# Optimization experiments

Measured on AMD Instinct MI355X. Metric: run time of the kernel, lower is better.

Reference implementation:

```python
import jax, jax.numpy as jnp
import numpy as np

N_NODES = 50000
N_EDGES = 1600000
IN_FEAT = 128
HEADS = 8
OUT_FEAT = 16


def setup_inputs() -> dict:
    key = jax.random.key(0)
    ks = jax.random.split(key, 8)
    feat = jax.random.normal(ks[0], (N_NODES, IN_FEAT), dtype=jnp.float32)
    src = jax.random.randint(ks[1], (N_EDGES,), 0, N_NODES, dtype=jnp.int32)
    dst = jax.random.randint(ks[2], (N_EDGES,), 0, N_NODES, dtype=jnp.int32)
    eps = jax.random.normal(ks[3], (N_EDGES, HEADS), dtype=jnp.float32)
    # small init scale keeps exp(log_scale) numerically tame
    W_fc = jax.random.normal(ks[4], (IN_FEAT, HEADS * OUT_FEAT), dtype=jnp.float32) * 0.05
    W_post = jax.random.normal(ks[5], (OUT_FEAT, 4), dtype=jnp.float32) * 0.05
    b_post = jax.random.normal(ks[6], (4,), dtype=jnp.float32) * 0.05
    bias = jax.random.normal(ks[7], (HEADS, OUT_FEAT), dtype=jnp.float32) * 0.05
    return {"feat": feat, "src": src, "dst": dst, "eps": eps,
            "W_fc": W_fc, "W_post": W_post, "b_post": b_post, "bias": bias}


def reference(feat, src, dst, eps, W_fc, W_post, b_post, bias):
    N = feat.shape[0]
    # node projection: [N, H, F]
    h = (feat @ W_fc).reshape(N, HEADS, OUT_FEAT)
    # per-node posterior params: [N, H, 4] -> loc_l, loc_r, log_scale_l, log_scale_r
    post = jnp.einsum('nhf,fk->nhk', h, W_post) + b_post
    loc_l, loc_r, lsl, lsr = post[..., 0], post[..., 1], post[..., 2], post[..., 3]
    # per-edge score via reparameterized sample: [E, H]
    loc = loc_l[src] + loc_r[dst]
    log_scale = lsl[src] + lsr[dst]
    e = loc + jnp.exp(log_scale) * eps
    # edge softmax over incoming edges of each dst node (per head)
    m = jax.lax.stop_gradient(jax.ops.segment_max(e, dst, num_segments=N))
    ex = jnp.exp(e - m[dst])
    denom = jax.ops.segment_sum(ex, dst, num_segments=N)
    a = ex / denom[dst]
    # weighted aggregation: sum over in-edges of h[src] * a
    msg = h[src] * a[:, :, None]                     # [E, H, F]
    out = jax.ops.segment_sum(msg, dst, num_segments=N)  # [N, H, F]
    out = out + bias[None]
    return out
```

## Files before the change

kernel.cpp:

```cpp
#include <hip/hip_runtime.h>
#include <hip/hip_fp16.h>

#define IN_FEAT 128
#define HEADS 8
#define OUT_FEAT 16
#define HF 128
#define BSHIFT 6
#define BNODES 64
#define NBMAX 1024
#define CHUNK 8192

__global__ __launch_bounds__(256) void gemm_post_kernel(
    const float* __restrict__ feat, const float* __restrict__ W_fc,
    const float* __restrict__ W_post, const float* __restrict__ b_post,
    __half* __restrict__ hbuf, float* __restrict__ post, int N)
{
    __shared__ float4 lds4[32 * 32];
    float* lds = (float*)lds4;
    const int tid = threadIdx.x;
    const int node_base = blockIdx.x * 32;

    const float4* f4 = (const float4*)feat;
    for (int i = tid; i < 32 * 32; i += 256) {
        int n = i >> 5, k4 = i & 31;
        int gn = node_base + n;
        float4 v = make_float4(0.f, 0.f, 0.f, 0.f);
        if (gn < N) v = f4[gn * 32 + k4];
        lds4[i] = v;
    }
    __syncthreads();

    const int cg = tid & 31, ng = tid >> 5;
    const int n0 = ng * 4;
    float acc[4][4];
#pragma unroll
    for (int i = 0; i < 4; i++) acc[i][0] = acc[i][1] = acc[i][2] = acc[i][3] = 0.f;

    const float4* W4 = (const float4*)W_fc;
#pragma unroll 4
    for (int k = 0; k < 128; ++k) {
        float4 w = W4[k * 32 + cg];
#pragma unroll
        for (int i = 0; i < 4; i++) {
            float f = lds[(n0 + i) * 128 + k];
            acc[i][0] += f * w.x; acc[i][1] += f * w.y;
            acc[i][2] += f * w.z; acc[i][3] += f * w.w;
        }
    }
    __half2* hb2 = (__half2*)hbuf;
#pragma unroll
    for (int i = 0; i < 4; i++) {
        int gn = node_base + n0 + i;
        if (gn < N) {
            union { uint2 u; __half2 h[2]; } pk;
            pk.h[0] = __floats2half2_rn(acc[i][0], acc[i][1]);
            pk.h[1] = __floats2half2_rn(acc[i][2], acc[i][3]);
            *(uint2*)&hb2[gn * 64 + cg * 2] = pk.u;
        }
    }
    __syncthreads();
#pragma unroll
    for (int i = 0; i < 4; i++)
        lds4[(n0 + i) * 32 + cg] = make_float4(acc[i][0], acc[i][1], acc[i][2], acc[i][3]);
    __syncthreads();

    {
        int n = tid >> 3, h = tid & 7;
        float p0 = b_post[0], p1 = b_post[1], p2 = b_post[2], p3 = b_post[3];
#pragma unroll
        for (int f = 0; f < 16; ++f) {
            float v = lds[n * 128 + h * 16 + f];
            p0 += v * W_post[f * 4 + 0];
            p1 += v * W_post[f * 4 + 1];
            p2 += v * W_post[f * 4 + 2];
            p3 += v * W_post[f * 4 + 3];
        }
        int gn = node_base + n;
        if (gn < N) {
            post[gn * 32 + 0 * 8 + h] = p0;
            post[gn * 32 + 1 * 8 + h] = p1;
            post[gn * 32 + 2 * 8 + h] = p2;
            post[gn * 32 + 3 * 8 + h] = p3;
        }
    }
}

__global__ __launch_bounds__(256) void bucket_hist_kernel(
    const int* __restrict__ dst, int* __restrict__ bucket_tot, int E, int nb)
{
    __shared__ int cnt[NBMAX];
    const int tid = threadIdx.x;
    for (int i = tid; i < nb; i += 256) cnt[i] = 0;
    __syncthreads();
    const int stride = gridDim.x * 256;
    for (int g = blockIdx.x * 256 + tid; g < E; g += stride)
        atomicAdd(&cnt[dst[g] >> BSHIFT], 1);
    __syncthreads();
    for (int i = tid; i < nb; i += 256) {
        int c = cnt[i];
        if (c) atomicAdd(&bucket_tot[i], c);
    }
}

__global__ __launch_bounds__(256) void bucket_scan_kernel(
    const int* __restrict__ bucket_tot, int* __restrict__ bucket_base,
    int* __restrict__ bucket_cursor, int nb, int E)
{
    __shared__ int sd[256];
    const int tid = threadIdx.x;
    int v[4]; int s = 0;
#pragma unroll
    for (int k = 0; k < 4; ++k) {
        int i = tid * 4 + k;
        v[k] = (i < nb) ? bucket_tot[i] : 0;
        s += v[k];
    }
    sd[tid] = s;
    __syncthreads();
    for (int off = 1; off < 256; off <<= 1) {
        int t = (tid >= off) ? sd[tid - off] : 0;
        __syncthreads();
        sd[tid] += t;
        __syncthreads();
    }
    int excl = sd[tid] - s;
#pragma unroll
    for (int k = 0; k < 4; ++k) {
        int i = tid * 4 + k;
        if (i < nb) { bucket_base[i] = excl; bucket_cursor[i] = excl; }
        excl += v[k];
    }
    if (tid == 0) bucket_base[nb] = E;
}

__global__ __launch_bounds__(256) void bucket_scatter_kernel(
    const int* __restrict__ src, const int* __restrict__ dst,
    int* __restrict__ bucket_cursor, uint2* __restrict__ recs, int E, int nb)
{
    __shared__ int cnt[NBMAX];
    __shared__ int base[NBMAX];
    const int tid = threadIdx.x;
    for (int i = tid; i < nb; i += 256) cnt[i] = 0;
    __syncthreads();
    const int e0 = blockIdx.x * CHUNK;
    const int e1 = min(e0 + CHUNK, E);
    for (int e = e0 + tid; e < e1; e += 256)
        atomicAdd(&cnt[dst[e] >> BSHIFT], 1);
    __syncthreads();
    for (int i = tid; i < nb; i += 256) {
        int c = cnt[i];
        base[i] = c ? atomicAdd(&bucket_cursor[i], c) : 0;
        cnt[i] = 0;
    }
    __syncthreads();
    for (int e = e0 + tid; e < e1; e += 256) {
        int d = dst[e];
        int b = d >> BSHIFT;
        int slot = base[b] + atomicAdd(&cnt[b], 1);
        recs[slot] = make_uint2((unsigned)e,
                                ((unsigned)src[e] << BSHIFT) | (unsigned)(d & (BNODES - 1)));
    }
}

__global__ __launch_bounds__(256) void bucket_csr_kernel(
    const uint2* __restrict__ recs, const int* __restrict__ bucket_base,
    int* __restrict__ offsets, uint2* __restrict__ csr, int N, int E)
{
    __shared__ int ncnt[BNODES];
    __shared__ int snc[BNODES];
    const int b = blockIdx.x, tid = threadIdx.x;
    const int node_lo = b << BSHIFT;
    const int rlo = bucket_base[b], rhi = bucket_base[b + 1];
    const int gn = node_lo + tid;

    if (tid < BNODES) ncnt[tid] = 0;
    __syncthreads();
    for (int r = rlo + tid; r < rhi; r += 256)
        atomicAdd(&ncnt[recs[r].y & (BNODES - 1u)], 1);
    __syncthreads();
    if (tid < BNODES) snc[tid] = ncnt[tid];
    __syncthreads();
    for (int off = 1; off < BNODES; off <<= 1) {
        int t = (tid < BNODES && tid >= off) ? snc[tid - off] : 0;
        __syncthreads();
        if (tid < BNODES) snc[tid] += t;
        __syncthreads();
    }
    int excl = (tid < BNODES) ? snc[tid] - ncnt[tid] : 0;
    if (tid < BNODES && gn < N) offsets[gn] = rlo + excl;
    if (b == 0 && tid == 0) offsets[N] = E;
    __syncthreads();
    if (tid < BNODES) ncnt[tid] = excl;
    __syncthreads();

    for (int r = rlo + tid; r < rhi; r += 256) {
        uint2 rec = recs[r];
        int dl = (int)(rec.y & (BNODES - 1u));
        unsigned s = rec.y >> BSHIFT;
        int slot = rlo + atomicAdd(&ncnt[dl], 1);
        csr[slot] = make_uint2(rec.x, s);
    }
}

__global__ __launch_bounds__(256) void agg_kernel(
    const uint2* __restrict__ csr, const int* __restrict__ offsets,
    const float* __restrict__ post, const float* __restrict__ eps,
    const __half* __restrict__ hbuf, const float* __restrict__ bias,
    float* __restrict__ out, int N)
{
    const int lane = threadIdx.x & 63;
    const int d = blockIdx.x * 4 + (threadIdx.x >> 6);
    if (d >= N) return;
    const int start = offsets[d];
    const int deg = offsets[d + 1] - start;
    const int j = lane >> 3, hh = lane & 7;
    const int h = j;
    const float dl  = post[d * 32 + 8 + hh];
    const float dls = post[d * 32 + 24 + hh];

    float2 acc = make_float2(0.f, 0.f);
    float dsum = 0.f;

    int c = 0;
    for (; c + 8 <= deg; c += 8) {
        uint2 rec = csr[start + c + j];
        int e = (int)rec.x, s = (int)rec.y;
        float ll = post[s * 32 + hh];
        float sl = post[s * 32 + 16 + hh];
        float ep = eps[(size_t)e * 8 + hh];
        float ex = __expf((ll + dl) + __expf(sl + dls) * ep);
#pragma unroll
        for (int jj = 0; jj < 8; ++jj) {
            float a = __shfl(ex, jj * 8 + h, 64);
            int  sj = __shfl(s, jj * 8, 64);
            float2 hv = __half22float2(((const __half2*)(hbuf + (size_t)sj * HF))[lane]);
            acc.x += a * hv.x;
            acc.y += a * hv.y;
            dsum += a;
        }
    }
    if (c < deg) {
        int jc = deg - c;
        uint2 rec = csr[start + c + min(j, jc - 1)];
        int e = (int)rec.x, s = (int)rec.y;
        float ll = post[s * 32 + hh];
        float sl = post[s * 32 + 16 + hh];
        float ep = eps[(size_t)e * 8 + hh];
        float ex = (j < jc) ? __expf((ll + dl) + __expf(sl + dls) * ep) : 0.f;
        for (int jj = 0; jj < jc; ++jj) {
            float a = __shfl(ex, jj * 8 + h, 64);
            int  sj = __shfl(s, jj * 8, 64);
            float2 hv = __half22float2(((const __half2*)(hbuf + (size_t)sj * HF))[lane]);
            acc.x += a * hv.x;
            acc.y += a * hv.y;
            dsum += a;
        }
    }

    float inv = (dsum > 0.f) ? 1.f / dsum : 0.f;
    float2 bv = ((const float2*)bias)[lane];
    float2 o = make_float2(acc.x * inv + bv.x, acc.y * inv + bv.y);
    ((float2*)out)[(size_t)d * 64 + lane] = o;
}

extern "C" void kernel_launch(void* const* d_in, const int* in_sizes, int n_in,
                              void* d_out, int out_size, void* d_ws, size_t ws_size,
                              hipStream_t stream)
{
    const float* feat   = (const float*)d_in[0];
    const int*   src    = (const int*)d_in[1];
    const int*   dst    = (const int*)d_in[2];
    const float* eps    = (const float*)d_in[3];
    const float* W_fc   = (const float*)d_in[4];
    const float* W_post = (const float*)d_in[5];
    const float* b_post = (const float*)d_in[6];
    const float* bias   = (const float*)d_in[7];
    float* out = (float*)d_out;

    const int N = in_sizes[0] / IN_FEAT;
    const int E = in_sizes[1];
    const int nb = (N + BNODES - 1) >> BSHIFT;

    char* p = (char*)d_ws;
    auto alloc = [&](size_t bytes) {
        char* r = p;
        p += (bytes + 255) & ~size_t(255);
        return r;
    };
    __half* hbuf    = (__half*)alloc((size_t)N * HF * 2);
    float*  post    = (float*)alloc((size_t)N * 32 * 4);
    int*    offsets = (int*)alloc((size_t)(N + 1) * 4);
    int*    bucket_tot    = (int*)alloc((size_t)(NBMAX + 1) * 4);
    int*    bucket_base   = (int*)alloc((size_t)(NBMAX + 1) * 4);
    int*    bucket_cursor = (int*)alloc((size_t)(NBMAX + 1) * 4);
    uint2*  recs    = (uint2*)alloc((size_t)E * 8);
    uint2*  csr     = (uint2*)alloc((size_t)E * 8);

    hipMemsetAsync(bucket_tot, 0, (size_t)nb * 4, stream);

    gemm_post_kernel<<<(N + 31) / 32, 256, 0, stream>>>(feat, W_fc, W_post, b_post,
                                                        hbuf, post, N);
    bucket_hist_kernel<<<512, 256, 0, stream>>>(dst, bucket_tot, E, nb);
    bucket_scan_kernel<<<1, 256, 0, stream>>>(bucket_tot, bucket_base,
                                              bucket_cursor, nb, E);
    bucket_scatter_kernel<<<(E + CHUNK - 1) / CHUNK, 256, 0, stream>>>(
        src, dst, bucket_cursor, recs, E, nb);
    bucket_csr_kernel<<<nb, 256, 0, stream>>>(recs, bucket_base, offsets, csr, N, E);
    agg_kernel<<<(N + 3) / 4, 256, 0, stream>>>(csr, offsets, post, eps, hbuf,
                                                bias, out, N);
}
```

Baseline: 333.4 us.

## Fuse GEMM with bucket scatter and sort per-bucket edges inside aggregation

Runs the edge bucket scatter and the node projection GEMM as disjoint block ranges of a single launch, so the two independent jobs overlap. It drops the separate CSR-building kernel. The aggregation kernel now takes one 64-node bucket per block, builds a local permutation of that bucket's records in shared memory, and accumulates all 8 nodes per wave in registers. This avoids writing and re-reading a full CSR array and saves a launch, at the cost of more shared memory, a larger register footprint, and fewer, heavier aggregation blocks that may load-balance poorly.

```diff
diff --git a/kernel.cpp b/kernel.cpp
--- a/kernel.cpp
+++ b/kernel.cpp
@@ -8,17 +8,96 @@
 #define BSHIFT 6
 #define BNODES 64
 #define NBMAX 1024
-#define CHUNK 8192
-
-__global__ __launch_bounds__(256) void gemm_post_kernel(
+#define CHUNK 4096
+#define PCAP 4096
+
+__global__ __launch_bounds__(256) void bucket_hist_kernel(
+    const int* __restrict__ dst, int* __restrict__ bucket_tot, int E, int nb)
+{
+    __shared__ int cnt[NBMAX];
+    const int tid = threadIdx.x;
+    for (int i = tid; i < nb; i += 256) cnt[i] = 0;
+    __syncthreads();
+    const int stride = gridDim.x * 256;
+    for (int g = blockIdx.x * 256 + tid; g < E; g += stride)
+        atomicAdd(&cnt[dst[g] >> BSHIFT], 1);
+    __syncthreads();
+    for (int i = tid; i < nb; i += 256) {
+        int c = cnt[i];
+        if (c) atomicAdd(&bucket_tot[i], c);
+    }
+}
+
+__global__ __launch_bounds__(256) void bucket_scan_kernel(
+    const int* __restrict__ bucket_tot, int* __restrict__ bucket_base,
+    int* __restrict__ bucket_cursor, int nb, int E)
+{
+    __shared__ int sd[256];
+    const int tid = threadIdx.x;
+    int v[4]; int s = 0;
+#pragma unroll
+    for (int k = 0; k < 4; ++k) {
+        int i = tid * 4 + k;
+        v[k] = (i < nb) ? bucket_tot[i] : 0;
+        s += v[k];
+    }
+    sd[tid] = s;
+    __syncthreads();
+    for (int off = 1; off < 256; off <<= 1) {
+        int t = (tid >= off) ? sd[tid - off] : 0;
+        __syncthreads();
+        sd[tid] += t;
+        __syncthreads();
+    }
+    int excl = sd[tid] - s;
+#pragma unroll
+    for (int k = 0; k < 4; ++k) {
+        int i = tid * 4 + k;
+        if (i < nb) { bucket_base[i] = excl; bucket_cursor[i] = excl; }
+        excl += v[k];
+    }
+    if (tid == 0) bucket_base[nb] = E;
+}
+
+__global__ __launch_bounds__(256) void gemm_scatter_kernel(
     const float* __restrict__ feat, const float* __restrict__ W_fc,
     const float* __restrict__ W_post, const float* __restrict__ b_post,
-    __half* __restrict__ hbuf, float* __restrict__ post, int N)
+    __half* __restrict__ hbuf, float* __restrict__ post, int N,
+    const int* __restrict__ src, const int* __restrict__ dst,
+    int* __restrict__ bucket_cursor, uint2* __restrict__ recs, int E, int nb,
+    int SB)
 {
     __shared__ float4 lds4[32 * 32];
+    const int tid = threadIdx.x;
+
+    if (blockIdx.x < SB) {
+        int* cnt  = (int*)lds4;
+        int* base = cnt + NBMAX;
+        for (int i = tid; i < nb; i += 256) cnt[i] = 0;
+        __syncthreads();
+        const int e0 = blockIdx.x * CHUNK;
+        const int e1 = min(e0 + CHUNK, E);
+        for (int e = e0 + tid; e < e1; e += 256)
+            atomicAdd(&cnt[dst[e] >> BSHIFT], 1);
+        __syncthreads();
+        for (int i = tid; i < nb; i += 256) {
+            int c = cnt[i];
+            base[i] = c ? atomicAdd(&bucket_cursor[i], c) : 0;
+            cnt[i] = 0;
+        }
+        __syncthreads();
+        for (int e = e0 + tid; e < e1; e += 256) {
+            int d = dst[e];
+            int b = d >> BSHIFT;
+            int slot = base[b] + atomicAdd(&cnt[b], 1);
+            recs[slot] = make_uint2((unsigned)e,
+                                    ((unsigned)src[e] << BSHIFT) | (unsigned)(d & (BNODES - 1)));
+        }
+        return;
+    }
+
     float* lds = (float*)lds4;
-    const int tid = threadIdx.x;
-    const int node_base = blockIdx.x * 32;
+    const int node_base = (blockIdx.x - SB) * 32;
 
     const float4* f4 = (const float4*)feat;
     for (int i = tid; i < 32 * 32; i += 256) {
@@ -85,182 +164,120 @@
     }
 }
 
-__global__ __launch_bounds__(256) void bucket_hist_kernel(
-    const int* __restrict__ dst, int* __restrict__ bucket_tot, int E, int nb)
-{
-    __shared__ int cnt[NBMAX];
-    const int tid = threadIdx.x;
-    for (int i = tid; i < nb; i += 256) cnt[i] = 0;
-    __syncthreads();
-    const int stride = gridDim.x * 256;
-    for (int g = blockIdx.x * 256 + tid; g < E; g += stride)
-        atomicAdd(&cnt[dst[g] >> BSHIFT], 1);
-    __syncthreads();
-    for (int i = tid; i < nb; i += 256) {
-        int c = cnt[i];
-        if (c) atomicAdd(&bucket_tot[i], c);
-    }
-}
-
-__global__ __launch_bounds__(256) void bucket_scan_kernel(
-    const int* __restrict__ bucket_tot, int* __restrict__ bucket_base,
-    int* __restrict__ bucket_cursor, int nb, int E)
-{
-    __shared__ int sd[256];
-    const int tid = threadIdx.x;
-    int v[4]; int s = 0;
-#pragma unroll
-    for (int k = 0; k < 4; ++k) {
-        int i = tid * 4 + k;
-        v[k] = (i < nb) ? bucket_tot[i] : 0;
-        s += v[k];
-    }
-    sd[tid] = s;
-    __syncthreads();
-    for (int off = 1; off < 256; off <<= 1) {
-        int t = (tid >= off) ? sd[tid - off] : 0;
-        __syncthreads();
-        sd[tid] += t;
-        __syncthreads();
-    }
-    int excl = sd[tid] - s;
-#pragma unroll
-    for (int k = 0; k < 4; ++k) {
-        int i = tid * 4 + k;
-        if (i < nb) { bucket_base[i] = excl; bucket_cursor[i] = excl; }
-        excl += v[k];
-    }
-    if (tid == 0) bucket_base[nb] = E;
-}
-
-__global__ __launch_bounds__(256) void bucket_scatter_kernel(
-    const int* __restrict__ src, const int* __restrict__ dst,
-    int* __restrict__ bucket_cursor, uint2* __restrict__ recs, int E, int nb)
-{
-    __shared__ int cnt[NBMAX];
-    __shared__ int base[NBMAX];
-    const int tid = threadIdx.x;
-    for (int i = tid; i < nb; i += 256) cnt[i] = 0;
-    __syncthreads();
-    const int e0 = blockIdx.x * CHUNK;
-    const int e1 = min(e0 + CHUNK, E);
-    for (int e = e0 + tid; e < e1; e += 256)
-        atomicAdd(&cnt[dst[e] >> BSHIFT], 1);
-    __syncthreads();
-    for (int i = tid; i < nb; i += 256) {
-        int c = cnt[i];
-        base[i] = c ? atomicAdd(&bucket_cursor[i], c) : 0;
-        cnt[i] = 0;
-    }
-    __syncthreads();
-    for (int e = e0 + tid; e < e1; e += 256) {
-        int d = dst[e];
-        int b = d >> BSHIFT;
-        int slot = base[b] + atomicAdd(&cnt[b], 1);
-        recs[slot] = make_uint2((unsigned)e,
-                                ((unsigned)src[e] << BSHIFT) | (unsigned)(d & (BNODES - 1)));
-    }
-}
-
-__global__ __launch_bounds__(256) void bucket_csr_kernel(
+__global__ __launch_bounds__(512) void agg_kernel(
     const uint2* __restrict__ recs, const int* __restrict__ bucket_base,
-    int* __restrict__ offsets, uint2* __restrict__ csr, int N, int E)
-{
+    const float* __restrict__ post, const float* __restrict__ eps,
+    const __half* __restrict__ hbuf, const float* __restrict__ bias,
+    float* __restrict__ out, int N)
+{
+    __shared__ unsigned short perm[PCAP];
     __shared__ int ncnt[BNODES];
-    __shared__ int snc[BNODES];
+    __shared__ int offs[BNODES];
+    __shared__ int cur[BNODES];
+
     const int b = blockIdx.x, tid = threadIdx.x;
     const int node_lo = b << BSHIFT;
     const int rlo = bucket_base[b], rhi = bucket_base[b + 1];
-    const int gn = node_lo + tid;
-
-    if (tid < BNODES) ncnt[tid] = 0;
-    __syncthreads();
-    for (int r = rlo + tid; r < rhi; r += 256)
-        atomicAdd(&ncnt[recs[r].y & (BNODES - 1u)], 1);
-    __syncthreads();
-    if (tid < BNODES) snc[tid] = ncnt[tid];
-    __syncthreads();
-    for (int off = 1; off < BNODES; off <<= 1) {
-        int t = (tid < BNODES && tid >= off) ? snc[tid - off] : 0;
-        __syncthreads();
-        if (tid < BNODES) snc[tid] += t;
-        __syncthreads();
-    }
-    int excl = (tid < BNODES) ? snc[tid] - ncnt[tid] : 0;
-    if (tid < BNODES && gn < N) offsets[gn] = rlo + excl;
-    if (b == 0 && tid == 0) offsets[N] = E;
-    __syncthreads();
-    if (tid < BNODES) ncnt[tid] = excl;
-    __syncthreads();
-
-    for (int r = rlo + tid; r < rhi; r += 256) {
-        uint2 rec = recs[r];
-        int dl = (int)(rec.y & (BNODES - 1u));
-        unsigned s = rec.y >> BSHIFT;
-        int slot = rlo + atomicAdd(&ncnt[dl], 1);
-        csr[slot] = make_uint2(rec.x, s);
-    }
-}
-
-__global__ __launch_bounds__(256) void agg_kernel(
-    const uint2* __restrict__ csr, const int* __restrict__ offsets,
-    const float* __restrict__ post, const float* __restrict__ eps,
-    const __half* __restrict__ hbuf, const float* __restrict__ bias,
-    float* __restrict__ out, int N)
-{
-    const int lane = threadIdx.x & 63;
-    const int d = blockIdx.x * 4 + (threadIdx.x >> 6);
-    if (d >= N) return;
-    const int start = offsets[d];
-    const int deg = offsets[d + 1] - start;
+    const int T = rhi - rlo;
+    const int w = tid >> 6, lane = tid & 63;
     const int j = lane >> 3, hh = lane & 7;
-    const int h = j;
-    const float dl  = post[d * 32 + 8 + hh];
-    const float dls = post[d * 32 + 24 + hh];
-
-    float2 acc = make_float2(0.f, 0.f);
-    float dsum = 0.f;
-
-    int c = 0;
-    for (; c + 8 <= deg; c += 8) {
-        uint2 rec = csr[start + c + j];
-        int e = (int)rec.x, s = (int)rec.y;
-        float ll = post[s * 32 + hh];
-        float sl = post[s * 32 + 16 + hh];
-        float ep = eps[(size_t)e * 8 + hh];
-        float ex = __expf((ll + dl) + __expf(sl + dls) * ep);
-#pragma unroll
-        for (int jj = 0; jj < 8; ++jj) {
-            float a = __shfl(ex, jj * 8 + h, 64);
-            int  sj = __shfl(s, jj * 8, 64);
-            float2 hv = __half22float2(((const __half2*)(hbuf + (size_t)sj * HF))[lane]);
-            acc.x += a * hv.x;
-            acc.y += a * hv.y;
-            dsum += a;
-        }
-    }
-    if (c < deg) {
-        int jc = deg - c;
-        uint2 rec = csr[start + c + min(j, jc - 1)];
-        int e = (int)rec.x, s = (int)rec.y;
-        float ll = post[s * 32 + hh];
-        float sl = post[s * 32 + 16 + hh];
-        float ep = eps[(size_t)e * 8 + hh];
-        float ex = (j < jc) ? __expf((ll + dl) + __expf(sl + dls) * ep) : 0.f;
-        for (int jj = 0; jj < jc; ++jj) {
-            float a = __shfl(ex, jj * 8 + h, 64);
-            int  sj = __shfl(s, jj * 8, 64);
-            float2 hv = __half22float2(((const __half2*)(hbuf + (size_t)sj * HF))[lane]);
-            acc.x += a * hv.x;
-            acc.y += a * hv.y;
-            dsum += a;
-        }
-    }
-
-    float inv = (dsum > 0.f) ? 1.f / dsum : 0.f;
-    float2 bv = ((const float2*)bias)[lane];
-    float2 o = make_float2(acc.x * inv + bv.x, acc.y * inv + bv.y);
-    ((float2*)out)[(size_t)d * 64 + lane] = o;
+
+    float2 acc[8];
+    float dsum[8];
+#pragma unroll
+    for (int i = 0; i < 8; i++) { acc[i] = make_float2(0.f, 0.f); dsum[i] = 0.f; }
+
+    for (int cb = 0; cb < T; cb += PCAP) {
+        const int Tc = min(PCAP, T - cb);
+        const uint2* rbase = recs + rlo + cb;
+
+        if (tid < BNODES) ncnt[tid] = 0;
+        __syncthreads();
+        for (int r = tid; r < Tc; r += 512)
+            atomicAdd(&ncnt[rbase[r].y & (BNODES - 1u)], 1);
+        __syncthreads();
+        if (tid < 64) {
+            int v = ncnt[tid];
+            int s = v;
+#pragma unroll
+            for (int off = 1; off < 64; off <<= 1) {
+                int t = __shfl_up(s, off, 64);
+                if (lane >= off) s += t;
+            }
+            offs[tid] = s - v;
+            cur[tid]  = s - v;
+        }
+        __syncthreads();
+        for (int r = tid; r < Tc; r += 512) {
+            int dl = (int)(rbase[r].y & (BNODES - 1u));
+            int slot = atomicAdd(&cur[dl], 1);
+            perm[slot] = (unsigned short)r;
+        }
+        __syncthreads();
+
+#pragma unroll
+        for (int i = 0; i < 8; i++) {
+            const int n = (i << 3) | w;
+            const int cn = ncnt[n];
+            if (cn == 0) continue;
+            const int o = offs[n];
+            const int gn = node_lo + n;
+            float dlr = 0.f, dls = 0.f;
+            if (gn < N) { dlr = post[gn * 32 + 8 + hh]; dls = post[gn * 32 + 24 + hh]; }
+
+            int c = 0;
+            for (; c + 8 <= cn; c += 8) {
+                int pidx = perm[o + c + j];
+                uint2 rec = rbase[pidx];
+                int e = (int)rec.x, s = (int)(rec.y >> BSHIFT);
+                float ll = post[s * 32 + hh];
+                float sl = post[s * 32 + 16 + hh];
+                float ep = eps[(size_t)e * 8 + hh];
+                float ex = __expf((ll + dlr) + __expf(sl + dls) * ep);
+#pragma unroll
+                for (int jj = 0; jj < 8; ++jj) {
+                    float a = __shfl(ex, jj * 8 + j, 64);
+                    int  sj = __shfl(s, jj * 8, 64);
+                    float2 hv = __half22float2(((const __half2*)(hbuf + (size_t)sj * HF))[lane]);
+                    acc[i].x += a * hv.x;
+                    acc[i].y += a * hv.y;
+                    dsum[i] += a;
+                }
+            }
+            if (c < cn) {
+                int jc = cn - c;
+                int pidx = perm[o + c + min(j, jc - 1)];
+                uint2 rec = rbase[pidx];
+                int e = (int)rec.x, s = (int)(rec.y >> BSHIFT);
+                float ll = post[s * 32 + hh];
+                float sl = post[s * 32 + 16 + hh];
+                float ep = eps[(size_t)e * 8 + hh];
+                float ex = (j < jc) ? __expf((ll + dlr) + __expf(sl + dls) * ep) : 0.f;
+                for (int jj = 0; jj < jc; ++jj) {
+                    float a = __shfl(ex, jj * 8 + j, 64);
+                    int  sj = __shfl(s, jj * 8, 64);
+                    float2 hv = __half22float2(((const __half2*)(hbuf + (size_t)sj * HF))[lane]);
+                    acc[i].x += a * hv.x;
+                    acc[i].y += a * hv.y;
+                    dsum[i] += a;
+                }
+            }
+        }
+        __syncthreads();
+    }
+
+    const float2 bv = ((const float2*)bias)[lane];
+    float2* out2 = (float2*)out;
+#pragma unroll
+    for (int i = 0; i < 8; i++) {
+        int n = (i << 3) | w;
+        int gn = node_lo + n;
+        if (gn < N) {
+            float inv = (dsum[i] > 0.f) ? 1.f / dsum[i] : 0.f;
+            out2[(size_t)gn * 64 + lane] = make_float2(acc[i].x * inv + bv.x,
+                                                       acc[i].y * inv + bv.y);
+        }
+    }
 }
 
 extern "C" void kernel_launch(void* const* d_in, const int* in_sizes, int n_in,
@@ -280,6 +297,8 @@
     const int N = in_sizes[0] / IN_FEAT;
     const int E = in_sizes[1];
     const int nb = (N + BNODES - 1) >> BSHIFT;
+    const int SB = (E + CHUNK - 1) / CHUNK;
+    const int GB = (N + 31) / 32;
 
     char* p = (char*)d_ws;
     auto alloc = [&](size_t bytes) {
@@ -289,23 +308,19 @@
     };
     __half* hbuf    = (__half*)alloc((size_t)N * HF * 2);
     float*  post    = (float*)alloc((size_t)N * 32 * 4);
-    int*    offsets = (int*)alloc((size_t)(N + 1) * 4);
     int*    bucket_tot    = (int*)alloc((size_t)(NBMAX + 1) * 4);
     int*    bucket_base   = (int*)alloc((size_t)(NBMAX + 1) * 4);
     int*    bucket_cursor = (int*)alloc((size_t)(NBMAX + 1) * 4);
     uint2*  recs    = (uint2*)alloc((size_t)E * 8);
-    uint2*  csr     = (uint2*)alloc((size_t)E * 8);
 
     hipMemsetAsync(bucket_tot, 0, (size_t)nb * 4, stream);
 
-    gemm_post_kernel<<<(N + 31) / 32, 256, 0, stream>>>(feat, W_fc, W_post, b_post,
-                                                        hbuf, post, N);
     bucket_hist_kernel<<<512, 256, 0, stream>>>(dst, bucket_tot, E, nb);
     bucket_scan_kernel<<<1, 256, 0, stream>>>(bucket_tot, bucket_base,
                                               bucket_cursor, nb, E);
-    bucket_scatter_kernel<<<(E + CHUNK - 1) / CHUNK, 256, 0, stream>>>(
-        src, dst, bucket_cursor, recs, E, nb);
-    bucket_csr_kernel<<<nb, 256, 0, stream>>>(recs, bucket_base, offsets, csr, N, E);
-    agg_kernel<<<(N + 3) / 4, 256, 0, stream>>>(csr, offsets, post, eps, hbuf,
-                                                bias, out, N);
-}
+    gemm_scatter_kernel<<<SB + GB, 256, 0, stream>>>(
+        feat, W_fc, W_post, b_post, hbuf, post, N,
+        src, dst, bucket_cursor, recs, E, nb, SB);
+    agg_kernel<<<nb, 512, 0, stream>>>(recs, bucket_base, post, eps, hbuf,
+                                       bias, out, N);
+}
```

New measurement: 371.7 us. 11.5% more time.
